# Performance work log

Measured on AMD Instinct MI355X. Metric: run time of the kernel, lower is better.

The kernel has to match this reference:

```python
import jax, jax.numpy as jnp
import numpy as np
import math

D_MODEL = 1024
HEAD_DIM = 256
GAMMA = 0.9


def setup_inputs() -> dict:
    key = jax.random.key(0)
    k1, k2, k3, k4 = jax.random.split(key, 4)
    B, L = 4, 4096
    x = jax.random.normal(k1, (B, L, D_MODEL), dtype=jnp.float32)
    s = 1.0 / math.sqrt(D_MODEL)
    W_Q = jax.random.normal(k2, (HEAD_DIM, D_MODEL), dtype=jnp.float32) * s
    W_K = jax.random.normal(k3, (HEAD_DIM, D_MODEL), dtype=jnp.float32) * s
    W_V = jax.random.normal(k4, (HEAD_DIM, D_MODEL), dtype=jnp.float32) * s
    return {"x": x, "W_Q": W_Q, "W_K": W_K, "W_V": W_V}


def _decay_mask(L: int, gamma: float) -> jnp.ndarray:
    # D[i,j] = gamma^(i-j) if i >= j else 0
    idx = jnp.arange(L)
    diff = idx[:, None] - idx[None, :]
    return jnp.where(diff >= 0, jnp.power(jnp.float32(gamma), diff.astype(jnp.float32)), 0.0)


def reference(x, W_Q, W_K, W_V):
    B, L, _ = x.shape
    Q = jnp.einsum('bld,hd->blh', x, W_Q)  # (B,L,H)
    K = jnp.einsum('bld,hd->blh', x, W_K)
    V = jnp.einsum('bld,hd->blh', x, W_V)
    D = _decay_mask(L, GAMMA)  # (L,L)
    scores = jnp.einsum('bih,bjh->bij', Q, K) * D[None, :, :]
    scores = scores / jnp.sqrt(jnp.float32(HEAD_DIM))
    return jnp.einsum('bij,bjh->bih', scores, V)  # (B,L,H)
```

## Files before the change

### kernel.cpp

```cpp
#include <hip/hip_runtime.h>

typedef unsigned short u16;
typedef unsigned int u32;
typedef __attribute__((ext_vector_type(8))) short bf16x8;
typedef __attribute__((ext_vector_type(4))) float f32x4;
typedef __attribute__((ext_vector_type(4))) unsigned short u16x4;

#define DEVI __device__ __forceinline__
#define AS1 __attribute__((address_space(1)))
#define AS3 __attribute__((address_space(3)))

constexpr float L2GAMMA = -0.15200309344504997f;
constexpr float INV_SQRT_H = 0.0625f;

DEVI u16 f2bf(float x) {
  union { float f; unsigned u; } v; v.f = x;
  unsigned r = v.u + 0x7FFFu + ((v.u >> 16) & 1u);
  return (u16)(r >> 16);
}

DEVI u32 pack2bf(float f0, float f1) {
  u32 u0 = __float_as_uint(f0) + 0x8000u;
  u32 u1 = __float_as_uint(f1) + 0x8000u;
  return __builtin_amdgcn_perm(u1, u0, 0x07060302u);
}

__global__ void cvt_w_kernel(const float4* __restrict__ wq, const float4* __restrict__ wk,
                             const float4* __restrict__ wv, u16x4* __restrict__ dst) {
  int i = blockIdx.x * blockDim.x + threadIdx.x;
  int w = i >> 16, off = i & 65535;
  const float4* s = (w == 0) ? wq : ((w == 1) ? wk : wv);
  float4 v = s[off];
  u16x4 o; o.x = f2bf(v.x); o.y = f2bf(v.y); o.z = f2bf(v.z); o.w = f2bf(v.w);
  dst[(w << 16) + off] = o;
}

__global__ __launch_bounds__(512, 2) void qkv_gemm_kernel(const float* __restrict__ Xf, const u16* __restrict__ Wb,
                                                          u16* __restrict__ Qb, u16* __restrict__ Kb,
                                                          u16* __restrict__ Vt) {
  __shared__ u16 Al[2][256 * 64];
  __shared__ u16 Bl[3][192 * 64];
  const int bid = blockIdx.x;
  const int xcd = bid & 7, seq = bid >> 3;
  const int m0 = (xcd * 8 + (seq >> 2)) * 256;
  const int n0 = (seq & 3) * 192;
  const int tid = threadIdx.x;
  const int wid = tid >> 6, lane = tid & 63;
  const int wm = wid >> 2, wn = wid & 3;
  const int lrow = lane & 15, lkg = lane >> 4;

  const int a_r = tid >> 4, a_s = tid & 15;
  const float* a_g = Xf + (size_t)(m0 + a_r) * 1024 + a_s * 4;
  const int a_wr = a_r * 64 + (((a_s >> 1) ^ (a_r & 7)) << 3) + ((a_s & 1) << 2);
  const int b_r = tid >> 3;
  const u16* b_g = Wb + (size_t)(n0 + b_r) * 1024 + (((tid & 7) ^ (b_r & 7)) << 3);

  float4 ar[8];

#define ALOAD(T) do { const float* g_ = a_g + (T) * 64; \
  _Pragma("unroll") for (int j_ = 0; j_ < 8; ++j_) \
    ar[j_] = *(const float4*)(g_ + (size_t)j_ * 32 * 1024); } while (0)

#define ACVT(P) do { \
  _Pragma("unroll") for (int j_ = 0; j_ < 8; ++j_) { \
    uint2 pk_; pk_.x = pack2bf(ar[j_].x, ar[j_].y); pk_.y = pack2bf(ar[j_].z, ar[j_].w); \
    *(uint2*)&Al[P][j_ * 2048 + a_wr] = pk_; } } while (0)

#define BSTAGE(T, BUF) do { const u16* g_ = b_g + (T) * 64; \
  _Pragma("unroll") for (int j_ = 0; j_ < 3; ++j_) \
    __builtin_amdgcn_global_load_lds((const AS1 void*)(g_ + (size_t)j_ * 64 * 1024), \
        (AS3 void*)&Bl[BUF][j_ * 4096 + tid * 8], 16, 0, 0); } while (0)

#define KKSTEP(KK, P, BQ) do { bf16x8 af_[8], bf_[3]; \
  const int ps_ = (((KK) * 4 + lkg) ^ (lrow & 7)) << 3; \
  _Pragma("unroll") for (int mf = 0; mf < 8; ++mf) \
    af_[mf] = *(const bf16x8*)&Al[P][(wm * 128 + mf * 16 + lrow) * 64 + ps_]; \
  _Pragma("unroll") for (int nf = 0; nf < 3; ++nf) \
    bf_[nf] = *(const bf16x8*)&Bl[BQ][(wn * 48 + nf * 16 + lrow) * 64 + ps_]; \
  __builtin_amdgcn_s_setprio(1); \
  _Pragma("unroll") for (int mf = 0; mf < 8; ++mf) \
    _Pragma("unroll") for (int nf = 0; nf < 3; ++nf) \
      acc[mf][nf] = __builtin_amdgcn_mfma_f32_16x16x32_bf16(af_[mf], bf_[nf], acc[mf][nf], 0, 0, 0); \
  __builtin_amdgcn_s_setprio(0); } while (0)

  f32x4 acc[8][3] = {};

  ALOAD(0);
  BSTAGE(0, 0); BSTAGE(1, 1);
  ACVT(0);
  asm volatile("s_waitcnt vmcnt(3) lgkmcnt(0)" ::: "memory");
  __builtin_amdgcn_s_barrier();

  int p = 0, bq = 0, wq = 2;
  for (int t = 0; t < 16; ++t) {
    if (t + 1 < 16) ALOAD(t + 1);
    if (t + 2 < 16) BSTAGE(t + 2, wq);
    KKSTEP(0, p, bq);
    if (t + 1 < 16) ACVT(p ^ 1);
    KKSTEP(1, p, bq);
    if (t < 15) {
      asm volatile("s_waitcnt vmcnt(3) lgkmcnt(0)" ::: "memory");
      __builtin_amdgcn_s_barrier();
    }
    p ^= 1;
    bq = (bq == 2) ? 0 : bq + 1;
    wq = (wq == 2) ? 0 : wq + 1;
  }

#pragma unroll
  for (int mf = 0; mf < 8; ++mf)
#pragma unroll
    for (int nf = 0; nf < 3; ++nf) {
      const int gm = m0 + wm * 128 + mf * 16 + lkg * 4;
      const int c = n0 + wn * 48 + nf * 16 + lrow;
      if (c < 512) {
        u16* Dst = (c < 256) ? Qb : Kb;
        const int cc = c & 255;
#pragma unroll
        for (int r = 0; r < 4; ++r) Dst[(size_t)(gm + r) * 256 + cc] = f2bf(acc[mf][nf][r]);
      } else {
        const int h = c - 512;
        const int bb = gm >> 12, l = gm & 4095;
        u16x4 pk;
        pk.x = f2bf(acc[mf][nf][0]); pk.y = f2bf(acc[mf][nf][1]);
        pk.z = f2bf(acc[mf][nf][2]); pk.w = f2bf(acc[mf][nf][3]);
        *(u16x4*)&Vt[((size_t)bb * 256 + h) * 4096 + l] = pk;
      }
    }
}

__global__ __launch_bounds__(256) void attn_kernel(const u16* __restrict__ Qb, const u16* __restrict__ Kb,
                                                   const u16* __restrict__ Vt, float* __restrict__ out) {
  __shared__ u16 Plds[32 * 72];
  const int raw = blockIdx.x;
  const int aid = (raw & 7) * 64 + (raw >> 3);
  const int b = aid >> 7;
  const int qt = aid & 127;
  const int qb = qt * 32;
  const int tid = threadIdx.x;
  const int wid = tid >> 6, lane = tid & 63;
  const int lrow = lane & 15, lkg = lane >> 4, lk = lkg * 8;
  const size_t bQK = (size_t)b * 4096 * 256;

  bf16x8 qf[2][8];
#pragma unroll
  for (int mf = 0; mf < 2; ++mf) {
    const u16* Qrow = Qb + bQK + (size_t)(qb + mf * 16 + lrow) * 256;
#pragma unroll
    for (int kf = 0; kf < 8; ++kf) qf[mf][kf] = *(const bf16x8*)&Qrow[kf * 32 + lk];
  }

  int kstart = qb - 256; if (kstart < 0) kstart = 0; kstart &= ~63;
  const int njt = (qb + 32 - kstart + 63) >> 6;

  f32x4 oacc[2][4] = {};

  for (int jt = 0; jt < njt; ++jt) {
    const int kb = kstart + jt * 64;
    f32x4 s[2] = {};
    const u16* Krow = Kb + bQK + (size_t)(kb + wid * 16 + lrow) * 256;
#pragma unroll
    for (int kf = 0; kf < 8; ++kf) {
      const bf16x8 kfr = *(const bf16x8*)&Krow[kf * 32 + lk];
      s[0] = __builtin_amdgcn_mfma_f32_16x16x32_bf16(qf[0][kf], kfr, s[0], 0, 0, 0);
      s[1] = __builtin_amdgcn_mfma_f32_16x16x32_bf16(qf[1][kf], kfr, s[1], 0, 0, 0);
    }
    const int kg = kb + wid * 16 + lrow;
#pragma unroll
    for (int mf = 0; mf < 2; ++mf) {
      const int qg = qb + mf * 16 + lkg * 4;
#pragma unroll
      for (int r = 0; r < 4; ++r) {
        const int d = qg + r - kg;
        const float pv = (d >= 0) ? s[mf][r] * exp2f((float)d * L2GAMMA) * INV_SQRT_H : 0.0f;
        Plds[(mf * 16 + lkg * 4 + r) * 72 + wid * 16 + lrow] = f2bf(pv);
      }
    }
    __syncthreads();
#pragma unroll
    for (int ks = 0; ks < 2; ++ks) {
      bf16x8 pa[2];
      pa[0] = *(const bf16x8*)&Plds[(lrow) * 72 + ks * 32 + lk];
      pa[1] = *(const bf16x8*)&Plds[(16 + lrow) * 72 + ks * 32 + lk];
#pragma unroll
      for (int nf = 0; nf < 4; ++nf) {
        const bf16x8 vb = *(const bf16x8*)&Vt[((size_t)b * 256 + wid * 64 + nf * 16 + lrow) * 4096 + kb + ks * 32 + lk];
        oacc[0][nf] = __builtin_amdgcn_mfma_f32_16x16x32_bf16(pa[0], vb, oacc[0][nf], 0, 0, 0);
        oacc[1][nf] = __builtin_amdgcn_mfma_f32_16x16x32_bf16(pa[1], vb, oacc[1][nf], 0, 0, 0);
      }
    }
    __syncthreads();
  }

#pragma unroll
  for (int mf = 0; mf < 2; ++mf) {
    float* obase = out + ((size_t)b * 4096 + qb + mf * 16 + lkg * 4) * 256 + wid * 64 + lrow;
#pragma unroll
    for (int nf = 0; nf < 4; ++nf)
#pragma unroll
      for (int r = 0; r < 4; ++r)
        obase[(size_t)r * 256 + nf * 16] = oacc[mf][nf][r];
  }
}

extern "C" void kernel_launch(void* const* d_in, const int* in_sizes, int n_in,
                              void* d_out, int out_size, void* d_ws, size_t ws_size,
                              hipStream_t stream) {
  const float* x  = (const float*)d_in[0];
  const float* wq = (const float*)d_in[1];
  const float* wk = (const float*)d_in[2];
  const float* wv = (const float*)d_in[3];
  float* out = (float*)d_out;
  char* ws = (char*)d_ws;
  u16* Wb = (u16*)(ws);
  u16* Qb = (u16*)(ws + (size_t)1572864);
  u16* Kb = (u16*)(ws + (size_t)9961472);
  u16* Vt = (u16*)(ws + (size_t)18350080);

  hipLaunchKernelGGL(cvt_w_kernel, dim3(768), dim3(256), 0, stream,
                     (const float4*)wq, (const float4*)wk, (const float4*)wv, (u16x4*)Wb);
  hipLaunchKernelGGL(qkv_gemm_kernel, dim3(256), dim3(512), 0, stream, x, Wb, Qb, Kb, Vt);
  hipLaunchKernelGGL(attn_kernel, dim3(512), dim3(256), 0, stream, Qb, Kb, Vt, out);
}
```

Before: 79.42 us.

## Pre-convert x to bf16 and simplify GEMM to register-staged double buffering

Adds a separate kernel that converts the fp32 input x to bf16 in workspace, so the QKV GEMM reads bf16 A tiles instead of converting fp32 in its inner loop. The GEMM loop moves from a triple-buffered B pipeline with direct global-to-LDS loads and hand-tuned waitcnts to simple register-staged double buffering with __syncthreads, and the launch-bounds occupancy hint drops from 2 to 1. This removes in-loop conversion work but adds an extra full pass over x (a 64 MB read and 32 MB write) plus a kernel launch, and the pipeline now overlaps less.

After: 100.6 us. 26.7% more time.

```diff
diff --git a/kernel.cpp b/kernel.cpp
--- a/kernel.cpp
+++ b/kernel.cpp
@@ -7,8 +7,6 @@
 typedef __attribute__((ext_vector_type(4))) unsigned short u16x4;
 
 #define DEVI __device__ __forceinline__
-#define AS1 __attribute__((address_space(1)))
-#define AS3 __attribute__((address_space(3)))
 
 constexpr float L2GAMMA = -0.15200309344504997f;
 constexpr float INV_SQRT_H = 0.0625f;
@@ -19,10 +17,13 @@
   return (u16)(r >> 16);
 }
 
-DEVI u32 pack2bf(float f0, float f1) {
-  u32 u0 = __float_as_uint(f0) + 0x8000u;
-  u32 u1 = __float_as_uint(f1) + 0x8000u;
-  return __builtin_amdgcn_perm(u1, u0, 0x07060302u);
+__global__ void cvt_x_kernel(const float4* __restrict__ src, u16x4* __restrict__ dst, int n4) {
+  int stride = gridDim.x * blockDim.x;
+  for (int i = blockIdx.x * blockDim.x + threadIdx.x; i < n4; i += stride) {
+    float4 v = src[i];
+    u16x4 o; o.x = f2bf(v.x); o.y = f2bf(v.y); o.z = f2bf(v.z); o.w = f2bf(v.w);
+    dst[i] = o;
+  }
 }
 
 __global__ void cvt_w_kernel(const float4* __restrict__ wq, const float4* __restrict__ wk,
@@ -35,11 +36,11 @@
   dst[(w << 16) + off] = o;
 }
 
-__global__ __launch_bounds__(512, 2) void qkv_gemm_kernel(const float* __restrict__ Xf, const u16* __restrict__ Wb,
+__global__ __launch_bounds__(512, 1) void qkv_gemm_kernel(const u16* __restrict__ Xb, const u16* __restrict__ Wb,
                                                           u16* __restrict__ Qb, u16* __restrict__ Kb,
                                                           u16* __restrict__ Vt) {
   __shared__ u16 Al[2][256 * 64];
-  __shared__ u16 Bl[3][192 * 64];
+  __shared__ u16 Bl[2][192 * 64];
   const int bid = blockIdx.x;
   const int xcd = bid & 7, seq = bid >> 3;
   const int m0 = (xcd * 8 + (seq >> 2)) * 256;
@@ -49,62 +50,68 @@
   const int wm = wid >> 2, wn = wid & 3;
   const int lrow = lane & 15, lkg = lane >> 4;
 
-  const int a_r = tid >> 4, a_s = tid & 15;
-  const float* a_g = Xf + (size_t)(m0 + a_r) * 1024 + a_s * 4;
-  const int a_wr = a_r * 64 + (((a_s >> 1) ^ (a_r & 7)) << 3) + ((a_s & 1) << 2);
-  const int b_r = tid >> 3;
-  const u16* b_g = Wb + (size_t)(n0 + b_r) * 1024 + (((tid & 7) ^ (b_r & 7)) << 3);
-
-  float4 ar[8];
-
-#define ALOAD(T) do { const float* g_ = a_g + (T) * 64; \
-  _Pragma("unroll") for (int j_ = 0; j_ < 8; ++j_) \
-    ar[j_] = *(const float4*)(g_ + (size_t)j_ * 32 * 1024); } while (0)
-
-#define ACVT(P) do { \
-  _Pragma("unroll") for (int j_ = 0; j_ < 8; ++j_) { \
-    uint2 pk_; pk_.x = pack2bf(ar[j_].x, ar[j_].y); pk_.y = pack2bf(ar[j_].z, ar[j_].w); \
-    *(uint2*)&Al[P][j_ * 2048 + a_wr] = pk_; } } while (0)
-
-#define BSTAGE(T, BUF) do { const u16* g_ = b_g + (T) * 64; \
-  _Pragma("unroll") for (int j_ = 0; j_ < 3; ++j_) \
-    __builtin_amdgcn_global_load_lds((const AS1 void*)(g_ + (size_t)j_ * 64 * 1024), \
-        (AS3 void*)&Bl[BUF][j_ * 4096 + tid * 8], 16, 0, 0); } while (0)
-
-#define KKSTEP(KK, P, BQ) do { bf16x8 af_[8], bf_[3]; \
-  const int ps_ = (((KK) * 4 + lkg) ^ (lrow & 7)) << 3; \
-  _Pragma("unroll") for (int mf = 0; mf < 8; ++mf) \
-    af_[mf] = *(const bf16x8*)&Al[P][(wm * 128 + mf * 16 + lrow) * 64 + ps_]; \
-  _Pragma("unroll") for (int nf = 0; nf < 3; ++nf) \
-    bf_[nf] = *(const bf16x8*)&Bl[BQ][(wn * 48 + nf * 16 + lrow) * 64 + ps_]; \
+  const int a_row = tid & 255;
+  const int a_jbase = tid >> 8;
+  uint4 ar[4], br[3];
+
+#define LOADA(T) do { \
+  _Pragma("unroll") for (int q_ = 0; q_ < 4; ++q_) { \
+    const int j_ = q_ * 2 + a_jbase; \
+    ar[q_] = *(const uint4*)(const void*)(Xb + (size_t)(m0 + a_row) * 1024 + (T) * 64 + j_ * 8); } \
+} while (0)
+
+#define LOADB(T) do { \
+  _Pragma("unroll") for (int q_ = 0; q_ < 3; ++q_) { \
+    const int L_ = q_ * 512 + tid; \
+    const int row_ = L_ % 192, j_ = L_ / 192; \
+    br[q_] = *(const uint4*)(const void*)(Wb + (size_t)(n0 + row_) * 1024 + (T) * 64 + j_ * 8); } \
+} while (0)
+
+#define WRITEA(P) do { \
+  _Pragma("unroll") for (int q_ = 0; q_ < 4; ++q_) { \
+    const int j_ = q_ * 2 + a_jbase; \
+    *(uint4*)&Al[P][a_row * 64 + ((j_ ^ (a_row & 7)) << 3)] = ar[q_]; } \
+} while (0)
+
+#define WRITEB(P) do { \
+  _Pragma("unroll") for (int q_ = 0; q_ < 3; ++q_) { \
+    const int L_ = q_ * 512 + tid; \
+    const int row_ = L_ % 192, j_ = L_ / 192; \
+    *(uint4*)&Bl[P][row_ * 64 + ((j_ ^ (row_ & 7)) << 3)] = br[q_]; } \
+} while (0)
+
+#define PHASE(C, P) do { \
+  bf16x8 af_[8], bf_[3]; \
+  _Pragma("unroll") for (int mf = 0; mf < 8; ++mf) { \
+    const int r_ = wm * 128 + mf * 16 + lrow; \
+    af_[mf] = *(const bf16x8*)&Al[P][r_ * 64 + ((((C) * 4 + lkg) ^ (r_ & 7)) << 3)]; } \
+  _Pragma("unroll") for (int nf = 0; nf < 3; ++nf) { \
+    const int r_ = wn * 48 + nf * 16 + lrow; \
+    bf_[nf] = *(const bf16x8*)&Bl[P][r_ * 64 + ((((C) * 4 + lkg) ^ (r_ & 7)) << 3)]; } \
   __builtin_amdgcn_s_setprio(1); \
   _Pragma("unroll") for (int mf = 0; mf < 8; ++mf) \
     _Pragma("unroll") for (int nf = 0; nf < 3; ++nf) \
       acc[mf][nf] = __builtin_amdgcn_mfma_f32_16x16x32_bf16(af_[mf], bf_[nf], acc[mf][nf], 0, 0, 0); \
-  __builtin_amdgcn_s_setprio(0); } while (0)
+  __builtin_amdgcn_s_setprio(0); \
+} while (0)
 
   f32x4 acc[8][3] = {};
 
-  ALOAD(0);
-  BSTAGE(0, 0); BSTAGE(1, 1);
-  ACVT(0);
-  asm volatile("s_waitcnt vmcnt(3) lgkmcnt(0)" ::: "memory");
-  __builtin_amdgcn_s_barrier();
-
-  int p = 0, bq = 0, wq = 2;
+  LOADA(0); LOADB(0);
+  WRITEA(0); WRITEB(0);
+  __syncthreads();
+
   for (int t = 0; t < 16; ++t) {
-    if (t + 1 < 16) ALOAD(t + 1);
-    if (t + 2 < 16) BSTAGE(t + 2, wq);
-    KKSTEP(0, p, bq);
-    if (t + 1 < 16) ACVT(p ^ 1);
-    KKSTEP(1, p, bq);
+    const int p = t & 1;
+    if (t < 15) { LOADA(t + 1); LOADB(t + 1); }
+    __builtin_amdgcn_sched_barrier(0);
+    PHASE(0, p);
+    PHASE(1, p);
+    __builtin_amdgcn_sched_barrier(0);
     if (t < 15) {
-      asm volatile("s_waitcnt vmcnt(3) lgkmcnt(0)" ::: "memory");
-      __builtin_amdgcn_s_barrier();
-    }
-    p ^= 1;
-    bq = (bq == 2) ? 0 : bq + 1;
-    wq = (wq == 2) ? 0 : wq + 1;
+      WRITEA(p ^ 1); WRITEB(p ^ 1);
+      __syncthreads();
+    }
   }
 
 #pragma unroll
@@ -212,13 +219,16 @@
   const float* wv = (const float*)d_in[3];
   float* out = (float*)d_out;
   char* ws = (char*)d_ws;
-  u16* Wb = (u16*)(ws);
-  u16* Qb = (u16*)(ws + (size_t)1572864);
-  u16* Kb = (u16*)(ws + (size_t)9961472);
-  u16* Vt = (u16*)(ws + (size_t)18350080);
-
+  u16* Xb = (u16*)(ws);
+  u16* Wb = (u16*)(ws + (size_t)33554432);
+  u16* Qb = (u16*)(ws + (size_t)35127296);
+  u16* Kb = (u16*)(ws + (size_t)43515904);
+  u16* Vt = (u16*)(ws + (size_t)51904512);
+
+  hipLaunchKernelGGL(cvt_x_kernel, dim3(2048), dim3(256), 0, stream,
+                     (const float4*)x, (u16x4*)Xb, 4194304);
   hipLaunchKernelGGL(cvt_w_kernel, dim3(768), dim3(256), 0, stream,
                      (const float4*)wq, (const float4*)wk, (const float4*)wv, (u16x4*)Wb);
-  hipLaunchKernelGGL(qkv_gemm_kernel, dim3(256), dim3(512), 0, stream, x, Wb, Qb, Kb, Vt);
+  hipLaunchKernelGGL(qkv_gemm_kernel, dim3(256), dim3(512), 0, stream, Xb, Wb, Qb, Kb, Vt);
   hipLaunchKernelGGL(attn_kernel, dim3(512), dim3(256), 0, stream, Qb, Kb, Vt, out);
 }
```

## Pre-pack X and W into MFMA fragment layout and drop LDS staging in GEMM

Applied to the files above, without the earlier changes.

Adds a separate kernel that converts x to bf16 in a fragment-ordered layout, and reworks the weight conversion to use the same layout. The QKV GEMM then loads MFMA operands straight from global memory without LDS, double buffering or barriers. This is meant to remove the in-loop fp32 conversion and LDS traffic. In exchange it writes and re-reads a 32MB bf16 copy of x and adds a launch, and each A fragment is fetched by the four N-tile blocks from global/L2 rather than reused through LDS.

Result: slower. 93.98 us (+18.3%).

```diff
diff --git a/kernel.cpp b/kernel.cpp
--- a/kernel.cpp
+++ b/kernel.cpp
@@ -7,8 +7,6 @@
 typedef __attribute__((ext_vector_type(4))) unsigned short u16x4;
 
 #define DEVI __device__ __forceinline__
-#define AS1 __attribute__((address_space(1)))
-#define AS3 __attribute__((address_space(3)))
 
 constexpr float L2GAMMA = -0.15200309344504997f;
 constexpr float INV_SQRT_H = 0.0625f;
@@ -19,92 +17,77 @@
   return (u16)(r >> 16);
 }
 
-DEVI u32 pack2bf(float f0, float f1) {
-  u32 u0 = __float_as_uint(f0) + 0x8000u;
-  u32 u1 = __float_as_uint(f1) + 0x8000u;
-  return __builtin_amdgcn_perm(u1, u0, 0x07060302u);
-}
-
-__global__ void cvt_w_kernel(const float4* __restrict__ wq, const float4* __restrict__ wk,
-                             const float4* __restrict__ wv, u16x4* __restrict__ dst) {
-  int i = blockIdx.x * blockDim.x + threadIdx.x;
-  int w = i >> 16, off = i & 65535;
-  const float4* s = (w == 0) ? wq : ((w == 1) ? wk : wv);
-  float4 v = s[off];
-  u16x4 o; o.x = f2bf(v.x); o.y = f2bf(v.y); o.z = f2bf(v.z); o.w = f2bf(v.w);
-  dst[(w << 16) + off] = o;
-}
-
-__global__ __launch_bounds__(512, 2) void qkv_gemm_kernel(const float* __restrict__ Xf, const u16* __restrict__ Wb,
-                                                          u16* __restrict__ Qb, u16* __restrict__ Kb,
-                                                          u16* __restrict__ Vt) {
-  __shared__ u16 Al[2][256 * 64];
-  __shared__ u16 Bl[3][192 * 64];
+
+__global__ void cvt_x_kernel(const float* __restrict__ x, u16* __restrict__ At) {
+  const int blk = blockIdx.x;
+  const int m16 = blk >> 3, quad = blk & 7;
+  const int tid = threadIdx.x;
+  const int lrow = tid & 15, lkg = (tid >> 4) & 3, q = tid >> 6;
+  const int k32 = quad * 4 + q;
+  const float* src = x + (size_t)(m16 * 16 + lrow) * 1024 + k32 * 32 + lkg * 8;
+  float4 v0 = *(const float4*)src;
+  float4 v1 = *(const float4*)(src + 4);
+  u16* dst = At + (size_t)(m16 * 32 + k32) * 512 + (size_t)(tid & 63) * 8;
+  u16x4 o0, o1;
+  o0.x = f2bf(v0.x); o0.y = f2bf(v0.y); o0.z = f2bf(v0.z); o0.w = f2bf(v0.w);
+  o1.x = f2bf(v1.x); o1.y = f2bf(v1.y); o1.z = f2bf(v1.z); o1.w = f2bf(v1.w);
+  *(u16x4*)dst = o0;
+  *(u16x4*)(dst + 4) = o1;
+}
+
+__global__ void cvt_w_kernel(const float* __restrict__ wq, const float* __restrict__ wk,
+                             const float* __restrict__ wv, u16* __restrict__ Wt) {
+  const int blk = blockIdx.x;
+  const int n16 = blk >> 3, quad = blk & 7;
+  const int tid = threadIdx.x;
+  const int lrow = tid & 15, lkg = (tid >> 4) & 3, q = tid >> 6;
+  const int k32 = quad * 4 + q;
+  const int row = n16 * 16 + lrow;
+  const int wsel = row >> 8, r = row & 255;
+  const float* w = (wsel == 0) ? wq : ((wsel == 1) ? wk : wv);
+  const float* src = w + (size_t)r * 1024 + k32 * 32 + lkg * 8;
+  float4 v0 = *(const float4*)src;
+  float4 v1 = *(const float4*)(src + 4);
+  u16* dst = Wt + (size_t)(n16 * 32 + k32) * 512 + (size_t)(tid & 63) * 8;
+  u16x4 o0, o1;
+  o0.x = f2bf(v0.x); o0.y = f2bf(v0.y); o0.z = f2bf(v0.z); o0.w = f2bf(v0.w);
+  o1.x = f2bf(v1.x); o1.y = f2bf(v1.y); o1.z = f2bf(v1.z); o1.w = f2bf(v1.w);
+  *(u16x4*)dst = o0;
+  *(u16x4*)(dst + 4) = o1;
+}
+
+__global__ __launch_bounds__(512) void qkv_gemm_kernel(const u16* __restrict__ At, const u16* __restrict__ Wt,
+                                                       u16* __restrict__ Qb, u16* __restrict__ Kb,
+                                                       u16* __restrict__ Vt) {
   const int bid = blockIdx.x;
   const int xcd = bid & 7, seq = bid >> 3;
-  const int m0 = (xcd * 8 + (seq >> 2)) * 256;
-  const int n0 = (seq & 3) * 192;
+  const int mp = xcd * 8 + (seq >> 2);
+  const int nt = seq & 3;
+  const int m0 = mp * 256, n0 = nt * 192;
   const int tid = threadIdx.x;
   const int wid = tid >> 6, lane = tid & 63;
   const int wm = wid >> 2, wn = wid & 3;
   const int lrow = lane & 15, lkg = lane >> 4;
 
-  const int a_r = tid >> 4, a_s = tid & 15;
-  const float* a_g = Xf + (size_t)(m0 + a_r) * 1024 + a_s * 4;
-  const int a_wr = a_r * 64 + (((a_s >> 1) ^ (a_r & 7)) << 3) + ((a_s & 1) << 2);
-  const int b_r = tid >> 3;
-  const u16* b_g = Wb + (size_t)(n0 + b_r) * 1024 + (((tid & 7) ^ (b_r & 7)) << 3);
-
-  float4 ar[8];
-
-#define ALOAD(T) do { const float* g_ = a_g + (T) * 64; \
-  _Pragma("unroll") for (int j_ = 0; j_ < 8; ++j_) \
-    ar[j_] = *(const float4*)(g_ + (size_t)j_ * 32 * 1024); } while (0)
-
-#define ACVT(P) do { \
-  _Pragma("unroll") for (int j_ = 0; j_ < 8; ++j_) { \
-    uint2 pk_; pk_.x = pack2bf(ar[j_].x, ar[j_].y); pk_.y = pack2bf(ar[j_].z, ar[j_].w); \
-    *(uint2*)&Al[P][j_ * 2048 + a_wr] = pk_; } } while (0)
-
-#define BSTAGE(T, BUF) do { const u16* g_ = b_g + (T) * 64; \
-  _Pragma("unroll") for (int j_ = 0; j_ < 3; ++j_) \
-    __builtin_amdgcn_global_load_lds((const AS1 void*)(g_ + (size_t)j_ * 64 * 1024), \
-        (AS3 void*)&Bl[BUF][j_ * 4096 + tid * 8], 16, 0, 0); } while (0)
-
-#define KKSTEP(KK, P, BQ) do { bf16x8 af_[8], bf_[3]; \
-  const int ps_ = (((KK) * 4 + lkg) ^ (lrow & 7)) << 3; \
-  _Pragma("unroll") for (int mf = 0; mf < 8; ++mf) \
-    af_[mf] = *(const bf16x8*)&Al[P][(wm * 128 + mf * 16 + lrow) * 64 + ps_]; \
-  _Pragma("unroll") for (int nf = 0; nf < 3; ++nf) \
-    bf_[nf] = *(const bf16x8*)&Bl[BQ][(wn * 48 + nf * 16 + lrow) * 64 + ps_]; \
-  __builtin_amdgcn_s_setprio(1); \
-  _Pragma("unroll") for (int mf = 0; mf < 8; ++mf) \
-    _Pragma("unroll") for (int nf = 0; nf < 3; ++nf) \
-      acc[mf][nf] = __builtin_amdgcn_mfma_f32_16x16x32_bf16(af_[mf], bf_[nf], acc[mf][nf], 0, 0, 0); \
-  __builtin_amdgcn_s_setprio(0); } while (0)
+  const u16* Ab = At + (size_t)((mp * 16 + wm * 8) * 32) * 512 + (size_t)lane * 8;
+  const u16* Bb = Wt + (size_t)((nt * 12 + wn * 3) * 32) * 512 + (size_t)lane * 8;
 
   f32x4 acc[8][3] = {};
 
-  ALOAD(0);
-  BSTAGE(0, 0); BSTAGE(1, 1);
-  ACVT(0);
-  asm volatile("s_waitcnt vmcnt(3) lgkmcnt(0)" ::: "memory");
-  __builtin_amdgcn_s_barrier();
-
-  int p = 0, bq = 0, wq = 2;
-  for (int t = 0; t < 16; ++t) {
-    if (t + 1 < 16) ALOAD(t + 1);
-    if (t + 2 < 16) BSTAGE(t + 2, wq);
-    KKSTEP(0, p, bq);
-    if (t + 1 < 16) ACVT(p ^ 1);
-    KKSTEP(1, p, bq);
-    if (t < 15) {
-      asm volatile("s_waitcnt vmcnt(3) lgkmcnt(0)" ::: "memory");
-      __builtin_amdgcn_s_barrier();
-    }
-    p ^= 1;
-    bq = (bq == 2) ? 0 : bq + 1;
-    wq = (wq == 2) ? 0 : wq + 1;
+#pragma unroll 2
+  for (int k32 = 0; k32 < 32; ++k32) {
+    bf16x8 a[8], b[3];
+#pragma unroll
+    for (int mf = 0; mf < 8; ++mf)
+      a[mf] = *(const bf16x8*)(Ab + (size_t)(mf * 32 + k32) * 512);
+#pragma unroll
+    for (int nf = 0; nf < 3; ++nf)
+      b[nf] = *(const bf16x8*)(Bb + (size_t)(nf * 32 + k32) * 512);
+#pragma unroll
+    for (int mf = 0; mf < 8; ++mf)
+#pragma unroll
+      for (int nf = 0; nf < 3; ++nf)
+        acc[mf][nf] = __builtin_amdgcn_mfma_f32_16x16x32_bf16(a[mf], b[nf], acc[mf][nf], 0, 0, 0);
   }
 
 #pragma unroll
@@ -212,13 +195,14 @@
   const float* wv = (const float*)d_in[3];
   float* out = (float*)d_out;
   char* ws = (char*)d_ws;
-  u16* Wb = (u16*)(ws);
-  u16* Qb = (u16*)(ws + (size_t)1572864);
-  u16* Kb = (u16*)(ws + (size_t)9961472);
-  u16* Vt = (u16*)(ws + (size_t)18350080);
-
-  hipLaunchKernelGGL(cvt_w_kernel, dim3(768), dim3(256), 0, stream,
-                     (const float4*)wq, (const float4*)wk, (const float4*)wv, (u16x4*)Wb);
-  hipLaunchKernelGGL(qkv_gemm_kernel, dim3(256), dim3(512), 0, stream, x, Wb, Qb, Kb, Vt);
+  u16* At = (u16*)(ws);
+  u16* Wt = (u16*)(ws + (size_t)33554432);
+  u16* Qb = (u16*)(ws + (size_t)35127296);
+  u16* Kb = (u16*)(ws + (size_t)43515904);
+  u16* Vt = (u16*)(ws + (size_t)51904512);
+
+  hipLaunchKernelGGL(cvt_x_kernel, dim3(8192), dim3(256), 0, stream, x, At);
+  hipLaunchKernelGGL(cvt_w_kernel, dim3(384), dim3(256), 0, stream, wq, wk, wv, Wt);
+  hipLaunchKernelGGL(qkv_gemm_kernel, dim3(256), dim3(512), 0, stream, At, Wt, Qb, Kb, Vt);
   hipLaunchKernelGGL(attn_kernel, dim3(512), dim3(256), 0, stream, Qb, Kb, Vt, out);
 }
```
